# Kernel optimization log

Measured on AMD Instinct MI355X. Metric: run time of the kernel, lower is better.

## Reference

```python
import jax, jax.numpy as jnp
import numpy as np

N_EXP = 8
TOP_K = 2
CAPACITY_FACTOR = 1.25


def setup_inputs() -> dict:
    key = jax.random.key(0)
    ks = jax.random.split(key, 5)
    B, T, D = 4, 1024, 1024
    H = 4 * D
    E = N_EXP
    x = jax.random.normal(ks[0], (B, T, D), jnp.float32)
    gate_w = jax.random.normal(ks[1], (D, E), jnp.float32) * 0.02
    c_fc = jax.random.normal(ks[2], (E, D, H), jnp.float32) * 0.02
    fc_bias = jnp.zeros((E, 1, H), jnp.float32)
    c_proj = jax.random.normal(ks[3], (E, H, D), jnp.float32) * 0.02
    proj_bias = jnp.zeros((E, 1, D), jnp.float32)
    return dict(x=x, gate_w=gate_w, c_fc=c_fc, fc_bias=fc_bias,
                c_proj=c_proj, proj_bias=proj_bias)


def reference(x, gate_w, c_fc, fc_bias, c_proj, proj_bias):
    B, T, D = x.shape
    n = B * T
    E, k = N_EXP, TOP_K
    cap = int(CAPACITY_FACTOR * n * k / E)  # expert capacity

    xt = x.reshape(n, D)

    # ---- Router ----
    logits = xt @ gate_w                                   # [n, E]
    top_logits, top_idx = jax.lax.top_k(logits, k)         # [n, k]
    # softmax over only the top-k experts (others set to -inf)
    masked = jnp.full_like(logits, -jnp.inf)
    masked = masked.at[jnp.arange(n)[:, None], top_idx].set(top_logits)
    router_probs = jax.nn.softmax(masked, axis=-1)         # [n, E]

    exp_mask = jax.nn.one_hot(top_idx, E, dtype=jnp.int32)  # [n, k, E]
    exp_mask = jnp.transpose(exp_mask, (1, 0, 2))           # [k, n, E]

    # rank of each token within its expert's batch (k=0 choices first)
    exp_rank = jnp.cumsum(exp_mask.reshape(k * n, E), axis=0) - 1
    exp_rank = exp_rank.reshape(k, n, E)

    # drop tokens exceeding capacity
    exp_mask = exp_mask * (exp_rank < cap).astype(jnp.int32)
    used_capacity = jnp.sum(exp_mask, axis=(0, 1))          # [E]

    exp_rank = jnp.sum(exp_mask * exp_rank, axis=-1)        # [k, n] slot index

    exp_weights = exp_mask.astype(x.dtype) * router_probs[None]  # [k, n, E]
    rank_oh = jax.nn.one_hot(exp_rank, cap, dtype=x.dtype)        # [k, n, cap]

    # combine weights [n, E, cap]
    cb_weight = jnp.einsum('kne,knc->nec', exp_weights, rank_oh)
    sec_mask = (cb_weight != 0).astype(x.dtype)             # dispatch mask

    # ---- Dispatch: one-hot matmul -> per-expert batches ----
    exp_batches = jnp.einsum('nec,nd->ecd', sec_mask, xt)   # [E, cap, D]

    # ---- Expert MLP (batched GEMMs, exact GELU, dropout=0/eval) ----
    h = jnp.einsum('ecd,edh->ech', exp_batches, c_fc) + fc_bias
    h = jax.nn.gelu(h, approximate=False)
    exp_out = jnp.einsum('ech,ehd->ecd', h, c_proj) + proj_bias  # [E, cap, D]

    # ---- Combine ----
    out = jnp.einsum('nec,ecd->nd', cb_weight, exp_out)     # [n, D]
    return out.reshape(B, T, D)
```

## Files before the change

### kernel.cpp

```cpp
#include <hip/hip_runtime.h>
#include <hip/hip_bf16.h>

typedef unsigned short u16;
typedef unsigned int u32;

#define N_TOK 4096
#define DIM   1024
#define HID   4096
#define N_EXP 8
#define CAP   1280

typedef short short8 __attribute__((ext_vector_type(8)));
typedef float f32x4 __attribute__((ext_vector_type(4)));

__device__ __forceinline__ u16 bf16rne(float f) {
    u32 u = __float_as_uint(f);
    u32 r = u + 0x7FFFu + ((u >> 16) & 1u);
    return (u16)(r >> 16);
}
__device__ __forceinline__ float bf2f(u16 h) {
    return __uint_as_float(((u32)h) << 16);
}

#define GLDS(gp, lp) __builtin_amdgcn_global_load_lds( \
    (const __attribute__((address_space(1))) void*)(gp), \
    (__attribute__((address_space(3))) void*)(lp), 16, 0, 0)

#define SBAR  asm volatile("s_barrier" ::: "memory")
#define LGKM0 asm volatile("s_waitcnt lgkmcnt(0)" ::: "memory")
#define VMW8  asm volatile("s_waitcnt vmcnt(8)" ::: "memory")
#define VMW5  asm volatile("s_waitcnt vmcnt(5)" ::: "memory")
#define VMW0  asm volatile("s_waitcnt vmcnt(0)" ::: "memory")

__global__ void router_kernel(const float* __restrict__ x,
                              const float* __restrict__ gw,
                              int* __restrict__ r_eidx,
                              float* __restrict__ r_w) {
    const int wave = threadIdx.x >> 6, lane = threadIdx.x & 63;
    const int t = blockIdx.x * 4 + wave;
    const float* xr = x + (size_t)t * DIM;
    float acc[8];
#pragma unroll
    for (int e = 0; e < 8; e++) acc[e] = 0.f;
#pragma unroll 4
    for (int i = 0; i < DIM / 64; i++) {
        int d = i * 64 + lane;
        float xv = xr[d];
        const float4* g = (const float4*)(gw + (size_t)d * 8);
        float4 g0 = g[0], g1 = g[1];
        acc[0] += xv * g0.x; acc[1] += xv * g0.y;
        acc[2] += xv * g0.z; acc[3] += xv * g0.w;
        acc[4] += xv * g1.x; acc[5] += xv * g1.y;
        acc[6] += xv * g1.z; acc[7] += xv * g1.w;
    }
#pragma unroll
    for (int e = 0; e < 8; e++) {
#pragma unroll
        for (int off = 32; off > 0; off >>= 1)
            acc[e] += __shfl_xor(acc[e], off, 64);
    }
    if (lane == 0) {
        int e0 = 0; float l0 = acc[0];
#pragma unroll
        for (int e = 1; e < 8; e++) if (acc[e] > l0) { l0 = acc[e]; e0 = e; }
        int e1 = -1; float l1 = -1e30f;
#pragma unroll
        for (int e = 0; e < 8; e++) if (e != e0 && acc[e] > l1) { l1 = acc[e]; e1 = e; }
        float z = __expf(l1 - l0);
        float inv = 1.f / (1.f + z);
        r_eidx[t] = e0; r_eidx[N_TOK + t] = e1;
        r_w[t] = inv;   r_w[N_TOK + t] = z * inv;
    }
}

__global__ void assign_kernel(const int* __restrict__ r_eidx,
                              int* __restrict__ assign_slot,
                              int* __restrict__ token_for_slot,
                              int* __restrict__ used) {
    const int tid = threadIdx.x;
    __shared__ int wtot[8][16];
    __shared__ int wbase[8][16];
    for (int i = tid; i < N_EXP * CAP; i += 1024) token_for_slot[i] = -1;

    int le[8], lr[8], cnt[8];
#pragma unroll
    for (int e = 0; e < 8; e++) cnt[e] = 0;
#pragma unroll
    for (int j = 0; j < 8; j++) {
        int e = r_eidx[tid * 8 + j];
        le[j] = e;
        int r = 0;
#pragma unroll
        for (int e2 = 0; e2 < 8; e2++)
            if (e == e2) { r = cnt[e2]; cnt[e2] = r + 1; }
        lr[j] = r;
    }
    const int lane = tid & 63, wv = tid >> 6;
    int excl[8];
#pragma unroll
    for (int e = 0; e < 8; e++) {
        int v = cnt[e], inc = v;
#pragma unroll
        for (int off = 1; off < 64; off <<= 1) {
            int u = __shfl_up(inc, off, 64);
            if (lane >= off) inc += u;
        }
        excl[e] = inc - v;
        if (lane == 63) wtot[e][wv] = inc;
    }
    __syncthreads();
    if (tid < 8) {
        int s = 0;
        for (int w = 0; w < 16; w++) { wbase[tid][w] = s; s += wtot[tid][w]; }
        used[tid] = s < CAP ? s : CAP;
    }
    __syncthreads();
#pragma unroll
    for (int j = 0; j < 8; j++) {
        int i = tid * 8 + j;
        int e = le[j];
        int b = 0;
#pragma unroll
        for (int e2 = 0; e2 < 8; e2++)
            if (e == e2) b = wbase[e2][wv] + excl[e2];
        int rank = b + lr[j];
        int tok = i & (N_TOK - 1);
        if (rank < CAP) {
            assign_slot[i] = rank;
            token_for_slot[e * CAP + rank] = tok;
        } else {
            assign_slot[i] = -1;
        }
    }
}

__global__ void gather_kernel(const float* __restrict__ x,
                              const int* __restrict__ token_for_slot,
                              u16* __restrict__ exp_batches) {
    const int s = blockIdx.x;
    const int tok = token_for_slot[s];
    const int d = threadIdx.x * 4;
    ushort4 o;
    if (tok >= 0) {
        float4 v = *(const float4*)(x + (size_t)tok * DIM + d);
        o = make_ushort4(bf16rne(v.x), bf16rne(v.y), bf16rne(v.z), bf16rne(v.w));
    } else {
        o = make_ushort4(0, 0, 0, 0);
    }
    *(ushort4*)(exp_batches + (size_t)s * DIM + d) = o;
}

__global__ __launch_bounds__(256) void transpose_cvt(
    const float* __restrict__ in, u16* __restrict__ out, int R, int C) {
    __shared__ float t[64][65];
    const int ez = blockIdx.z;
    in  += (size_t)ez * R * C;
    out += (size_t)ez * R * C;
    const int row0 = blockIdx.y * 64, col0 = blockIdx.x * 64;
    const int tid = threadIdx.x;
    {
        const int r = tid >> 2, cq = (tid & 3) * 16;
        const float* p = in + (size_t)(row0 + r) * C + col0 + cq;
        float4 v0 = ((const float4*)p)[0];
        float4 v1 = ((const float4*)p)[1];
        float4 v2 = ((const float4*)p)[2];
        float4 v3 = ((const float4*)p)[3];
        float tmp[16] = {v0.x, v0.y, v0.z, v0.w, v1.x, v1.y, v1.z, v1.w,
                         v2.x, v2.y, v2.z, v2.w, v3.x, v3.y, v3.z, v3.w};
#pragma unroll
        for (int j = 0; j < 16; j++) t[r][cq + j] = tmp[j];
    }
    __syncthreads();
    {
        const int oc = tid >> 2, h4 = (tid & 3) * 16;
        u16 o[16];
#pragma unroll
        for (int i = 0; i < 16; i++) o[i] = bf16rne(t[h4 + i][oc]);
        u16* q = out + (size_t)(col0 + oc) * R + row0 + h4;
        *(uint4*)q = *(const uint4*)&o[0];
        *(uint4*)(q + 8) = *(const uint4*)&o[8];
    }
}

template <int BM, bool DO_GELU>
__global__ __launch_bounds__(512, 2) void moe_gemm256(
    const u16* __restrict__ A, const u16* __restrict__ Bt,
    const float* __restrict__ bias, u16* __restrict__ C,
    const int* __restrict__ used, int N, int K) {
    constexpr int MI   = BM / 32;
    constexpr int ALW  = BM / 32;
    constexpr int BUFE = (BM + 256) * 64;
    constexpr int NROW = CAP / BM;
    __shared__ __align__(16) u16 lds[2 * BUFE];

    const int NT = K >> 6;
    const int bid = blockIdx.x;
    const int e = bid & 7;
    const int local = bid >> 3;
    const int row0 = (local % NROW) * BM;
    const int col0 = (local / NROW) * 256;
    if (row0 >= used[e]) return;

    A    += (size_t)e * CAP * K;
    Bt   += (size_t)e * N * K;
    bias += (size_t)e * N;
    C    += (size_t)e * CAP * N;

    const int tid = threadIdx.x;
    const int lane = tid & 63, wave = tid >> 6;
    const int mh   = wave >> 2;
    const int wv4  = wave & 3;
    const int wr   = mh * (BM / 2);
    const int wc64 = wv4 * 64;

    const int srow = lane >> 3;
    const int swz  = ((lane & 7) ^ srow) * 8;
    const int LW   = mh ? 8 : ALW;
    const int ro0  = wv4 * LW * 8;
    const u16* gsrc = (mh ? Bt + (size_t)(col0 + ro0 + srow) * K
                          : A  + (size_t)(row0 + ro0 + srow) * K) + swz;
    u16* dbase = lds + (mh ? BM * 64 : 0) + ro0 * 64;

    auto stage = [&](int buf, int kt) {
        u16* db = dbase + (size_t)buf * BUFE;
        const u16* sb = gsrc + kt;
        if (mh) {
#pragma unroll
            for (int i = 0; i < 8; ++i)
                GLDS(sb + (size_t)(i * 8) * K, db + i * 512);
        } else {
#pragma unroll
            for (int i = 0; i < ALW; ++i)
                GLDS(sb + (size_t)(i * 8) * K, db + i * 512);
        }
    };
    auto waitL = [&]() {
        if constexpr (ALW == 8) { VMW8; }
        else { if (mh) { VMW8; } else { VMW5; } }
    };

    f32x4 acc[MI][4];
#pragma unroll
    for (int i = 0; i < MI; i++)
#pragma unroll
        for (int j = 0; j < 4; j++) acc[i][j] = (f32x4){0.f, 0.f, 0.f, 0.f};

    stage(0, 0);
    stage(1, 64);
    waitL();
    SBAR;

    const int rrd = lane & 15, qrd = lane >> 4;
    const int k0 = ((qrd ^ (rrd & 7)) << 3);
    const int k1 = (((4 + qrd) ^ (rrd & 7)) << 3);
    const int aoff = (wr + rrd) * 64;
    const int boff = (wc64 + rrd) * 64;

    for (int t = 0; t < NT; ++t) {
        const u16* As = lds + (size_t)(t & 1) * BUFE;
        const u16* Bs = As + BM * 64;

        short8 bf0[4], bf1[4];
#pragma unroll
        for (int j = 0; j < 4; ++j) {
            bf0[j] = *(const short8*)(Bs + boff + j * 1024 + k0);
            bf1[j] = *(const short8*)(Bs + boff + j * 1024 + k1);
        }
#pragma unroll
        for (int i = 0; i < MI; ++i) {
            short8 a0 = *(const short8*)(As + aoff + i * 1024 + k0);
            short8 a1 = *(const short8*)(As + aoff + i * 1024 + k1);
            __builtin_amdgcn_s_setprio(1);
#pragma unroll
            for (int j = 0; j < 4; ++j)
                acc[i][j] = __builtin_amdgcn_mfma_f32_16x16x32_bf16(
                    a0, bf0[j], acc[i][j], 0, 0, 0);
#pragma unroll
            for (int j = 0; j < 4; ++j)
                acc[i][j] = __builtin_amdgcn_mfma_f32_16x16x32_bf16(
                    a1, bf1[j], acc[i][j], 0, 0, 0);
            __builtin_amdgcn_s_setprio(0);
        }

        if (t < NT - 1) {
            LGKM0;
            __builtin_amdgcn_sched_barrier(0);
            SBAR;
            if (t + 2 < NT) { stage(t & 1, (t + 2) * 64); waitL(); }
            else            { VMW0; }
            SBAR;
        }
    }

    const int cr = qrd * 4;
    const int cc = rrd;
    float bv[4];
#pragma unroll
    for (int j = 0; j < 4; ++j) bv[j] = bias[col0 + wc64 + j * 16 + cc];
#pragma unroll
    for (int i = 0; i < MI; ++i) {
#pragma unroll
        for (int r = 0; r < 4; ++r) {
            const int row = row0 + wr + i * 16 + cr + r;
            u16* cp = C + (size_t)row * N + col0 + wc64 + cc;
#pragma unroll
            for (int j = 0; j < 4; ++j) {
                float v = acc[i][j][r] + bv[j];
                if (DO_GELU) {
                    float u = 0.7978845608f * v * (1.f + 0.044715f * v * v);
                    v = v / (1.f + __expf(-2.f * u));
                }
                cp[j * 16] = bf16rne(v);
            }
        }
    }
}

__global__ void combine_kernel(const int* __restrict__ r_eidx,
                               const float* __restrict__ r_w,
                               const int* __restrict__ assign_slot,
                               const u16* __restrict__ exp_out,
                               float* __restrict__ out) {
    const int t = blockIdx.x;
    const int d = threadIdx.x * 4;
    const int e0 = r_eidx[t], e1 = r_eidx[N_TOK + t];
    const float w0 = r_w[t], w1 = r_w[N_TOK + t];
    const int s0 = assign_slot[t], s1 = assign_slot[N_TOK + t];
    float v0 = 0.f, v1 = 0.f, v2 = 0.f, v3 = 0.f;
    if (s0 >= 0) {
        const u16* p = exp_out + ((size_t)e0 * CAP + s0) * DIM + d;
        ushort4 q = *(const ushort4*)p;
        v0 += w0 * bf2f(q.x); v1 += w0 * bf2f(q.y);
        v2 += w0 * bf2f(q.z); v3 += w0 * bf2f(q.w);
    }
    if (s1 >= 0) {
        const u16* p = exp_out + ((size_t)e1 * CAP + s1) * DIM + d;
        ushort4 q = *(const ushort4*)p;
        v0 += w1 * bf2f(q.x); v1 += w1 * bf2f(q.y);
        v2 += w1 * bf2f(q.z); v3 += w1 * bf2f(q.w);
    }
    float4 o; o.x = v0; o.y = v1; o.z = v2; o.w = v3;
    *(float4*)(out + (size_t)t * DIM + d) = o;
}

extern "C" void kernel_launch(void* const* d_in, const int* in_sizes, int n_in,
                              void* d_out, int out_size, void* d_ws, size_t ws_size,
                              hipStream_t stream) {
    const float* x         = (const float*)d_in[0];
    const float* gate_w    = (const float*)d_in[1];
    const float* c_fc      = (const float*)d_in[2];
    const float* fc_bias   = (const float*)d_in[3];
    const float* c_proj    = (const float*)d_in[4];
    const float* proj_bias = (const float*)d_in[5];
    float* out = (float*)d_out;
    char* ws = (char*)d_ws;

    int*   r_eidx         = (int*)(ws + 0);
    float* r_w            = (float*)(ws + 32768);
    int*   assign_slot    = (int*)(ws + 65536);
    int*   token_for_slot = (int*)(ws + 98304);
    int*   used           = (int*)(ws + 139264);
    u16*   exp_batches    = (u16*)(ws + 163840);
    u16*   exp_out        = exp_batches;
    u16*   h              = (u16*)(ws + 21135360);
    u16*   Bt             = (u16*)(ws + 105021440);

    router_kernel<<<N_TOK / 4, 256, 0, stream>>>(x, gate_w, r_eidx, r_w);
    assign_kernel<<<1, 1024, 0, stream>>>(r_eidx, assign_slot, token_for_slot, used);
    gather_kernel<<<N_EXP * CAP, 256, 0, stream>>>(x, token_for_slot, exp_batches);

    transpose_cvt<<<dim3(HID / 64, DIM / 64, N_EXP), 256, 0, stream>>>(
        c_fc, Bt, DIM, HID);
    moe_gemm256<256, true><<<(CAP / 256) * (HID / 256) * N_EXP, 512, 0, stream>>>(
        exp_batches, Bt, fc_bias, h, used, HID, DIM);

    transpose_cvt<<<dim3(DIM / 64, HID / 64, N_EXP), 256, 0, stream>>>(
        c_proj, Bt, HID, DIM);
    moe_gemm256<160, false><<<(CAP / 160) * (DIM / 256) * N_EXP, 512, 0, stream>>>(
        h, Bt, proj_bias, exp_out, used, DIM, HID);

    combine_kernel<<<N_TOK, 256, 0, stream>>>(r_eidx, r_w, assign_slot, exp_out, out);
}
```

Measured before the change: 559.7 us.

## Make expert GEMM persistent over row tiles with cross-tile prefetch

The expert GEMM kernel now lets each block loop over several row tiles that share the same column tile, and prefetches the next tile's first K-slices during the tail of the current one. The first GEMM switches from 256-row tiles to 160-row tiles with four tiles per block, giving a fixed grid of 256 blocks. The aim is to cut tail effects and launch imbalance, reuse the B column tile's cache locality, and overlap tile transitions. In exchange there is less parallelism per launch, and load balance now depends on how many tokens each expert receives.

Measured after the change: 559.1 us. No clear change (-0.1%).

```diff
diff --git a/kernel.cpp b/kernel.cpp
--- a/kernel.cpp
+++ b/kernel.cpp
@@ -182,24 +182,31 @@
     }
 }
 
-template <int BM, bool DO_GELU>
-__global__ __launch_bounds__(512, 2) void moe_gemm256(
+template <int BM, int TPB, bool DO_GELU>
+__global__ __launch_bounds__(512, 2) void moe_gemmP(
     const u16* __restrict__ A, const u16* __restrict__ Bt,
     const float* __restrict__ bias, u16* __restrict__ C,
     const int* __restrict__ used, int N, int K) {
-    constexpr int MI   = BM / 32;
-    constexpr int ALW  = BM / 32;
-    constexpr int BUFE = (BM + 256) * 64;
-    constexpr int NROW = CAP / BM;
+    constexpr int MI    = BM / 32;
+    constexpr int ALW   = BM / 32;
+    constexpr int BUFE  = (BM + 256) * 64;
+    constexpr int NROWT = CAP / BM;
+    constexpr int RB    = NROWT / TPB;
     __shared__ __align__(16) u16 lds[2 * BUFE];
 
     const int NT = K >> 6;
     const int bid = blockIdx.x;
     const int e = bid & 7;
     const int local = bid >> 3;
-    const int row0 = (local % NROW) * BM;
-    const int col0 = (local / NROW) * 256;
-    if (row0 >= used[e]) return;
+    const int col0 = (local / RB) * 256;
+    const int rgrp = local % RB;
+
+    const int u = used[e];
+    int nact = 0;
+#pragma unroll
+    for (int q = 0; q < TPB; ++q)
+        if ((rgrp + q * RB) * BM < u) nact = q + 1;
+    if (nact == 0) return;
 
     A    += (size_t)e * CAP * K;
     Bt   += (size_t)e * N * K;
@@ -217,13 +224,15 @@
     const int swz  = ((lane & 7) ^ srow) * 8;
     const int LW   = mh ? 8 : ALW;
     const int ro0  = wv4 * LW * 8;
-    const u16* gsrc = (mh ? Bt + (size_t)(col0 + ro0 + srow) * K
-                          : A  + (size_t)(row0 + ro0 + srow) * K) + swz;
+    int row0 = rgrp * BM;
+    const size_t astep = (size_t)RB * BM * K;
+    const u16* gp = (mh ? Bt + (size_t)(col0 + ro0 + srow) * K
+                        : A  + (size_t)(row0 + ro0 + srow) * K) + swz;
+    const size_t nextoff = mh ? 0 : astep;
     u16* dbase = lds + (mh ? BM * 64 : 0) + ro0 * 64;
 
-    auto stage = [&](int buf, int kt) {
+    auto stage = [&](int buf, const u16* sb) {
         u16* db = dbase + (size_t)buf * BUFE;
-        const u16* sb = gsrc + kt;
         if (mh) {
 #pragma unroll
             for (int i = 0; i < 8; ++i)
@@ -239,80 +248,96 @@
         else { if (mh) { VMW8; } else { VMW5; } }
     };
 
-    f32x4 acc[MI][4];
-#pragma unroll
-    for (int i = 0; i < MI; i++)
-#pragma unroll
-        for (int j = 0; j < 4; j++) acc[i][j] = (f32x4){0.f, 0.f, 0.f, 0.f};
-
-    stage(0, 0);
-    stage(1, 64);
-    waitL();
-    SBAR;
-
     const int rrd = lane & 15, qrd = lane >> 4;
     const int k0 = ((qrd ^ (rrd & 7)) << 3);
     const int k1 = (((4 + qrd) ^ (rrd & 7)) << 3);
     const int aoff = (wr + rrd) * 64;
     const int boff = (wc64 + rrd) * 64;
-
-    for (int t = 0; t < NT; ++t) {
-        const u16* As = lds + (size_t)(t & 1) * BUFE;
-        const u16* Bs = As + BM * 64;
-
-        short8 bf0[4], bf1[4];
-#pragma unroll
-        for (int j = 0; j < 4; ++j) {
-            bf0[j] = *(const short8*)(Bs + boff + j * 1024 + k0);
-            bf1[j] = *(const short8*)(Bs + boff + j * 1024 + k1);
-        }
-#pragma unroll
-        for (int i = 0; i < MI; ++i) {
-            short8 a0 = *(const short8*)(As + aoff + i * 1024 + k0);
-            short8 a1 = *(const short8*)(As + aoff + i * 1024 + k1);
-            __builtin_amdgcn_s_setprio(1);
-#pragma unroll
-            for (int j = 0; j < 4; ++j)
-                acc[i][j] = __builtin_amdgcn_mfma_f32_16x16x32_bf16(
-                    a0, bf0[j], acc[i][j], 0, 0, 0);
-#pragma unroll
-            for (int j = 0; j < 4; ++j)
-                acc[i][j] = __builtin_amdgcn_mfma_f32_16x16x32_bf16(
-                    a1, bf1[j], acc[i][j], 0, 0, 0);
-            __builtin_amdgcn_s_setprio(0);
-        }
-
-        if (t < NT - 1) {
-            LGKM0;
-            __builtin_amdgcn_sched_barrier(0);
-            SBAR;
-            if (t + 2 < NT) { stage(t & 1, (t + 2) * 64); waitL(); }
-            else            { VMW0; }
-            SBAR;
-        }
-    }
-
     const int cr = qrd * 4;
     const int cc = rrd;
+
     float bv[4];
 #pragma unroll
     for (int j = 0; j < 4; ++j) bv[j] = bias[col0 + wc64 + j * 16 + cc];
-#pragma unroll
-    for (int i = 0; i < MI; ++i) {
-#pragma unroll
-        for (int r = 0; r < 4; ++r) {
-            const int row = row0 + wr + i * 16 + cr + r;
-            u16* cp = C + (size_t)row * N + col0 + wc64 + cc;
+
+    f32x4 acc[MI][4];
+
+    for (int tt = 0; ; ++tt) {
+#pragma unroll
+        for (int i = 0; i < MI; i++)
+#pragma unroll
+            for (int j = 0; j < 4; j++) acc[i][j] = (f32x4){0.f, 0.f, 0.f, 0.f};
+
+        if (tt == 0) { stage(0, gp); stage(1, gp + 64); }
+        waitL();
+        SBAR;
+
+        const bool hasnext = (tt + 1 < nact);
+
+        for (int t = 0; t < NT; ++t) {
+            const u16* As = lds + (size_t)(t & 1) * BUFE;
+            const u16* Bs = As + BM * 64;
+
+            short8 bf0[4], bf1[4];
 #pragma unroll
             for (int j = 0; j < 4; ++j) {
-                float v = acc[i][j][r] + bv[j];
-                if (DO_GELU) {
-                    float u = 0.7978845608f * v * (1.f + 0.044715f * v * v);
-                    v = v / (1.f + __expf(-2.f * u));
-                }
-                cp[j * 16] = bf16rne(v);
+                bf0[j] = *(const short8*)(Bs + boff + j * 1024 + k0);
+                bf1[j] = *(const short8*)(Bs + boff + j * 1024 + k1);
+            }
+#pragma unroll
+            for (int i = 0; i < MI; ++i) {
+                short8 a0 = *(const short8*)(As + aoff + i * 1024 + k0);
+                short8 a1 = *(const short8*)(As + aoff + i * 1024 + k1);
+                __builtin_amdgcn_s_setprio(1);
+#pragma unroll
+                for (int j = 0; j < 4; ++j)
+                    acc[i][j] = __builtin_amdgcn_mfma_f32_16x16x32_bf16(
+                        a0, bf0[j], acc[i][j], 0, 0, 0);
+#pragma unroll
+                for (int j = 0; j < 4; ++j)
+                    acc[i][j] = __builtin_amdgcn_mfma_f32_16x16x32_bf16(
+                        a1, bf1[j], acc[i][j], 0, 0, 0);
+                __builtin_amdgcn_s_setprio(0);
+            }
+
+            if (t < NT - 1) {
+                LGKM0;
+                __builtin_amdgcn_sched_barrier(0);
+                SBAR;
+                const int idx = t + 2;
+                if (idx < NT)     { stage(idx & 1, gp + idx * 64); waitL(); }
+                else if (hasnext) { stage(0, gp + nextoff); waitL(); }
+                else              { VMW0; }
+                SBAR;
+            } else if (hasnext) {
+                LGKM0;
+                __builtin_amdgcn_sched_barrier(0);
+                SBAR;
+                stage(1, gp + nextoff + 64);
             }
         }
+
+#pragma unroll
+        for (int i = 0; i < MI; ++i) {
+#pragma unroll
+            for (int r = 0; r < 4; ++r) {
+                const int row = row0 + wr + i * 16 + cr + r;
+                u16* cp = C + (size_t)row * N + col0 + wc64 + cc;
+#pragma unroll
+                for (int j = 0; j < 4; ++j) {
+                    float v = acc[i][j][r] + bv[j];
+                    if (DO_GELU) {
+                        float uu = 0.7978845608f * v * (1.f + 0.044715f * v * v);
+                        v = v / (1.f + __expf(-2.f * uu));
+                    }
+                    cp[j * 16] = bf16rne(v);
+                }
+            }
+        }
+
+        if (!hasnext) break;
+        gp += nextoff;
+        row0 += RB * BM;
     }
 }
 
@@ -371,12 +396,12 @@
 
     transpose_cvt<<<dim3(HID / 64, DIM / 64, N_EXP), 256, 0, stream>>>(
         c_fc, Bt, DIM, HID);
-    moe_gemm256<256, true><<<(CAP / 256) * (HID / 256) * N_EXP, 512, 0, stream>>>(
+    moe_gemmP<160, 4, true><<<256, 512, 0, stream>>>(
         exp_batches, Bt, fc_bias, h, used, HID, DIM);
 
     transpose_cvt<<<dim3(DIM / 64, HID / 64, N_EXP), 256, 0, stream>>>(
         c_proj, Bt, HID, DIM);
-    moe_gemm256<160, false><<<(CAP / 160) * (DIM / 256) * N_EXP, 512, 0, stream>>>(
+    moe_gemmP<160, 1, false><<<256, 512, 0, stream>>>(
         h, Bt, proj_bias, exp_out, used, DIM, HID);
 
     combine_kernel<<<N_TOK, 256, 0, stream>>>(r_eidx, r_w, assign_slot, exp_out, out);
```

## Persistent multi-tile MoE GEMMs with triple buffering and atomic fused combine

Applied to the files above, without the earlier changes.

Both expert GEMMs become fixed-grid (256 blocks) kernels where each block loops over several column tiles with a continuous three-stage LDS pipeline across tile boundaries. The second GEMM's epilogue scales results by router weights and atomically adds them straight into the zeroed fp32 output, which removes the bf16 exp_out buffer and the combine kernel. The first GEMM moves from 256-row to 160-row tiles. The atomics add contention and make summation order nondeterministic, and the memset is an extra launch.

New measurement: 565.9 us. About the same (+1.1%).

```diff
diff --git a/kernel.cpp b/kernel.cpp
--- a/kernel.cpp
+++ b/kernel.cpp
@@ -20,6 +20,9 @@
 }
 __device__ __forceinline__ float bf2f(u16 h) {
     return __uint_as_float(((u32)h) << 16);
+}
+__device__ __forceinline__ void atomAddF32(float* p, float v) {
+    asm volatile("global_atomic_add_f32 %0, %1, off" :: "v"(p), "v"(v) : "memory");
 }
 
 #define GLDS(gp, lp) __builtin_amdgcn_global_load_lds( \
@@ -74,7 +77,8 @@
 }
 
 __global__ void assign_kernel(const int* __restrict__ r_eidx,
-                              int* __restrict__ assign_slot,
+                              const float* __restrict__ r_w,
+                              float* __restrict__ wslot,
                               int* __restrict__ token_for_slot,
                               int* __restrict__ used) {
     const int tid = threadIdx.x;
@@ -126,10 +130,8 @@
         int rank = b + lr[j];
         int tok = i & (N_TOK - 1);
         if (rank < CAP) {
-            assign_slot[i] = rank;
             token_for_slot[e * CAP + rank] = tok;
-        } else {
-            assign_slot[i] = -1;
+            wslot[e * CAP + rank] = r_w[i];
         }
     }
 }
@@ -182,29 +184,34 @@
     }
 }
 
-template <int BM, bool DO_GELU>
-__global__ __launch_bounds__(512, 2) void moe_gemm256(
+template <int BM, int TPB, int NTILE, int EPI>
+__global__ __launch_bounds__(512, 2) void moe_gemmT(
     const u16* __restrict__ A, const u16* __restrict__ Bt,
-    const float* __restrict__ bias, u16* __restrict__ C,
-    const int* __restrict__ used, int N, int K) {
+    const float* __restrict__ bias, u16* __restrict__ Cb,
+    float* __restrict__ outF, const int* __restrict__ tfs_,
+    const float* __restrict__ wsl_, const int* __restrict__ used,
+    int N, int K) {
     constexpr int MI   = BM / 32;
     constexpr int ALW  = BM / 32;
     constexpr int BUFE = (BM + 256) * 64;
-    constexpr int NROW = CAP / BM;
-    __shared__ __align__(16) u16 lds[2 * BUFE];
-
-    const int NT = K >> 6;
+    constexpr int RB   = CAP / BM;
+    constexpr int NCG  = 32 / RB;
+    constexpr int LNT  = (NTILE == 16) ? 4 : 6;
+    constexpr int G    = TPB * NTILE;
+    __shared__ __align__(16) u16 lds[3 * BUFE];
+
     const int bid = blockIdx.x;
     const int e = bid & 7;
     const int local = bid >> 3;
-    const int row0 = (local % NROW) * BM;
-    const int col0 = (local / NROW) * 256;
+    const int rgrp = local % RB;
+    const int cg   = local / RB;
+    const int row0 = rgrp * BM;
     if (row0 >= used[e]) return;
 
     A    += (size_t)e * CAP * K;
     Bt   += (size_t)e * N * K;
     bias += (size_t)e * N;
-    C    += (size_t)e * CAP * N;
+    if constexpr (EPI == 1) Cb += (size_t)e * CAP * N;
 
     const int tid = threadIdx.x;
     const int lane = tid & 63, wave = tid >> 6;
@@ -215,15 +222,16 @@
 
     const int srow = lane >> 3;
     const int swz  = ((lane & 7) ^ srow) * 8;
-    const int LW   = mh ? 8 : ALW;
-    const int ro0  = wv4 * LW * 8;
-    const u16* gsrc = (mh ? Bt + (size_t)(col0 + ro0 + srow) * K
-                          : A  + (size_t)(row0 + ro0 + srow) * K) + swz;
-    u16* dbase = lds + (mh ? BM * 64 : 0) + ro0 * 64;
-
-    auto stage = [&](int buf, int kt) {
-        u16* db = dbase + (size_t)buf * BUFE;
-        const u16* sb = gsrc + kt;
+    const int ro0  = wv4 * (mh ? 8 : ALW) * 8;
+    const size_t segB = (size_t)NCG * 256 * K;
+    const u16* gp = (mh ? Bt + (size_t)(cg * 256 + ro0 + srow) * K
+                        : A  + (size_t)(row0 + ro0 + srow) * K) + swz;
+    u16* dwb = lds + (mh ? BM * 64 : 0) + ro0 * 64;
+
+    auto stage = [&](int g, int buf) {
+        const u16* sb = gp + (size_t)(g & (NTILE - 1)) * 64;
+        if (mh) sb += (size_t)(g >> LNT) * segB;
+        u16* db = dwb + (size_t)buf * BUFE;
         if (mh) {
 #pragma unroll
             for (int i = 0; i < 8; ++i)
@@ -234,30 +242,30 @@
                 GLDS(sb + (size_t)(i * 8) * K, db + i * 512);
         }
     };
-    auto waitL = [&]() {
-        if constexpr (ALW == 8) { VMW8; }
-        else { if (mh) { VMW8; } else { VMW5; } }
-    };
-
-    f32x4 acc[MI][4];
-#pragma unroll
-    for (int i = 0; i < MI; i++)
-#pragma unroll
-        for (int j = 0; j < 4; j++) acc[i][j] = (f32x4){0.f, 0.f, 0.f, 0.f};
-
-    stage(0, 0);
-    stage(1, 64);
-    waitL();
-    SBAR;
+    auto waitL = [&]() { if (mh) { VMW8; } else { VMW5; } };
 
     const int rrd = lane & 15, qrd = lane >> 4;
     const int k0 = ((qrd ^ (rrd & 7)) << 3);
     const int k1 = (((4 + qrd) ^ (rrd & 7)) << 3);
     const int aoff = (wr + rrd) * 64;
     const int boff = (wc64 + rrd) * 64;
-
-    for (int t = 0; t < NT; ++t) {
-        const u16* As = lds + (size_t)(t & 1) * BUFE;
+    const int cr = qrd * 4;
+    const int cc = rrd;
+
+    f32x4 acc[MI][4];
+#pragma unroll
+    for (int i = 0; i < MI; i++)
+#pragma unroll
+        for (int j = 0; j < 4; j++) acc[i][j] = (f32x4){0.f, 0.f, 0.f, 0.f};
+
+    stage(0, 0);
+    stage(1, 1);
+    waitL();
+    SBAR;
+
+    int bcur = 0, bst = 2, q = 0;
+    for (int g = 0; g < G; ++g) {
+        const u16* As = lds + bcur * BUFE;
         const u16* Bs = As + BM * 64;
 
         short8 bf0[4], bf1[4];
@@ -282,65 +290,71 @@
             __builtin_amdgcn_s_setprio(0);
         }
 
-        if (t < NT - 1) {
+        if (g < G - 1) {
             LGKM0;
             __builtin_amdgcn_sched_barrier(0);
             SBAR;
-            if (t + 2 < NT) { stage(t & 1, (t + 2) * 64); waitL(); }
-            else            { VMW0; }
+            if (g + 2 < G) {
+                stage(g + 2, bst);
+                waitL();
+                bst = (bst == 2) ? 0 : bst + 1;
+            } else {
+                VMW0;
+            }
             SBAR;
         }
-    }
-
-    const int cr = qrd * 4;
-    const int cc = rrd;
-    float bv[4];
-#pragma unroll
-    for (int j = 0; j < 4; ++j) bv[j] = bias[col0 + wc64 + j * 16 + cc];
-#pragma unroll
-    for (int i = 0; i < MI; ++i) {
-#pragma unroll
-        for (int r = 0; r < 4; ++r) {
-            const int row = row0 + wr + i * 16 + cr + r;
-            u16* cp = C + (size_t)row * N + col0 + wc64 + cc;
-#pragma unroll
-            for (int j = 0; j < 4; ++j) {
-                float v = acc[i][j][r] + bv[j];
-                if (DO_GELU) {
-                    float u = 0.7978845608f * v * (1.f + 0.044715f * v * v);
-                    v = v / (1.f + __expf(-2.f * u));
+        bcur = (bcur == 2) ? 0 : bcur + 1;
+
+        if ((g & (NTILE - 1)) == NTILE - 1) {
+            const int col0 = (cg + q * NCG) * 256;
+            if constexpr (EPI == 1) {
+                float bv[4];
+#pragma unroll
+                for (int j = 0; j < 4; ++j) bv[j] = bias[col0 + wc64 + j * 16 + cc];
+#pragma unroll
+                for (int i = 0; i < MI; ++i) {
+#pragma unroll
+                    for (int r = 0; r < 4; ++r) {
+                        const int row = row0 + wr + i * 16 + cr + r;
+                        u16* cp = Cb + (size_t)row * N + col0 + wc64 + cc;
+#pragma unroll
+                        for (int j = 0; j < 4; ++j) {
+                            float v = acc[i][j][r] + bv[j];
+                            float uu = 0.7978845608f * v * (1.f + 0.044715f * v * v);
+                            v = v / (1.f + __expf(-2.f * uu));
+                            cp[j * 16] = bf16rne(v);
+                        }
+                    }
                 }
-                cp[j * 16] = bf16rne(v);
+            } else {
+                const int* tfs = tfs_ + e * CAP;
+                const float* wsl = wsl_ + e * CAP;
+                float bv[4];
+#pragma unroll
+                for (int j = 0; j < 4; ++j) bv[j] = bias[col0 + wc64 + j * 16 + cc];
+#pragma unroll
+                for (int i = 0; i < MI; ++i) {
+#pragma unroll
+                    for (int r = 0; r < 4; ++r) {
+                        const int row = row0 + wr + i * 16 + cr + r;
+                        const int tok = tfs[row];
+                        if (tok >= 0) {
+                            const float w = wsl[row];
+                            float* op = outF + (size_t)tok * DIM + col0 + wc64 + cc;
+#pragma unroll
+                            for (int j = 0; j < 4; ++j)
+                                atomAddF32(op + j * 16, w * (acc[i][j][r] + bv[j]));
+                        }
+                    }
+                }
             }
-        }
-    }
-}
-
-__global__ void combine_kernel(const int* __restrict__ r_eidx,
-                               const float* __restrict__ r_w,
-                               const int* __restrict__ assign_slot,
-                               const u16* __restrict__ exp_out,
-                               float* __restrict__ out) {
-    const int t = blockIdx.x;
-    const int d = threadIdx.x * 4;
-    const int e0 = r_eidx[t], e1 = r_eidx[N_TOK + t];
-    const float w0 = r_w[t], w1 = r_w[N_TOK + t];
-    const int s0 = assign_slot[t], s1 = assign_slot[N_TOK + t];
-    float v0 = 0.f, v1 = 0.f, v2 = 0.f, v3 = 0.f;
-    if (s0 >= 0) {
-        const u16* p = exp_out + ((size_t)e0 * CAP + s0) * DIM + d;
-        ushort4 q = *(const ushort4*)p;
-        v0 += w0 * bf2f(q.x); v1 += w0 * bf2f(q.y);
-        v2 += w0 * bf2f(q.z); v3 += w0 * bf2f(q.w);
-    }
-    if (s1 >= 0) {
-        const u16* p = exp_out + ((size_t)e1 * CAP + s1) * DIM + d;
-        ushort4 q = *(const ushort4*)p;
-        v0 += w1 * bf2f(q.x); v1 += w1 * bf2f(q.y);
-        v2 += w1 * bf2f(q.z); v3 += w1 * bf2f(q.w);
-    }
-    float4 o; o.x = v0; o.y = v1; o.z = v2; o.w = v3;
-    *(float4*)(out + (size_t)t * DIM + d) = o;
+#pragma unroll
+            for (int i = 0; i < MI; i++)
+#pragma unroll
+                for (int j = 0; j < 4; j++) acc[i][j] = (f32x4){0.f, 0.f, 0.f, 0.f};
+            ++q;
+        }
+    }
 }
 
 extern "C" void kernel_launch(void* const* d_in, const int* in_sizes, int n_in,
@@ -357,27 +371,25 @@
 
     int*   r_eidx         = (int*)(ws + 0);
     float* r_w            = (float*)(ws + 32768);
-    int*   assign_slot    = (int*)(ws + 65536);
-    int*   token_for_slot = (int*)(ws + 98304);
-    int*   used           = (int*)(ws + 139264);
+    float* wslot          = (float*)(ws + 65536);
+    int*   token_for_slot = (int*)(ws + 106496);
+    int*   used           = (int*)(ws + 147456);
     u16*   exp_batches    = (u16*)(ws + 163840);
-    u16*   exp_out        = exp_batches;
     u16*   h              = (u16*)(ws + 21135360);
     u16*   Bt             = (u16*)(ws + 105021440);
 
+    hipMemsetAsync(out, 0, (size_t)N_TOK * DIM * sizeof(float), stream);
     router_kernel<<<N_TOK / 4, 256, 0, stream>>>(x, gate_w, r_eidx, r_w);
-    assign_kernel<<<1, 1024, 0, stream>>>(r_eidx, assign_slot, token_for_slot, used);
+    assign_kernel<<<1, 1024, 0, stream>>>(r_eidx, r_w, wslot, token_for_slot, used);
     gather_kernel<<<N_EXP * CAP, 256, 0, stream>>>(x, token_for_slot, exp_batches);
 
     transpose_cvt<<<dim3(HID / 64, DIM / 64, N_EXP), 256, 0, stream>>>(
         c_fc, Bt, DIM, HID);
-    moe_gemm256<256, true><<<(CAP / 256) * (HID / 256) * N_EXP, 512, 0, stream>>>(
-        exp_batches, Bt, fc_bias, h, used, HID, DIM);
+    moe_gemmT<160, 4, 16, 1><<<256, 512, 0, stream>>>(
+        exp_batches, Bt, fc_bias, h, nullptr, nullptr, nullptr, used, HID, DIM);
 
     transpose_cvt<<<dim3(DIM / 64, HID / 64, N_EXP), 256, 0, stream>>>(
         c_proj, Bt, HID, DIM);
-    moe_gemm256<160, false><<<(CAP / 160) * (DIM / 256) * N_EXP, 512, 0, stream>>>(
-        h, Bt, proj_bias, exp_out, used, DIM, HID);
-
-    combine_kernel<<<N_TOK, 256, 0, stream>>>(r_eidx, r_w, assign_slot, exp_out, out);
-}
+    moe_gemmT<160, 1, 64, 2><<<256, 512, 0, stream>>>(
+        h, Bt, proj_bias, nullptr, out, token_for_slot, wslot, used, DIM, HID);
+}
```
